# Performance work log

Hardware: AMD Instinct MI355X
Metric: run time of the kernel (lower is better)

The kernel has to match this reference:

```python
import jax, jax.numpy as jnp
import numpy as np
from jax import lax

ANCHOR_LENGTHS = (1.0, 2.0, 3.0, 4.0, 5.0, 7.0, 9.0)
B, C, LF = 8, 512, 8192
A = len(ANCHOR_LENGTHS)
PRE_K, POST_K = 600, 100          # pre/post NMS topk (propose defaults)
SCORE_TH, IOU_TH = 0.1, 0.5


def setup_inputs() -> dict:
    key = jax.random.key(0)
    ks = jax.random.split(key, 7)
    def n(k, shape, scale=1.0):
        return jax.random.normal(k, shape, dtype=jnp.float32) * scale
    return {
        "feat": n(ks[0], (B, C, LF)),
        "conv_w": n(ks[1], (C, C, 3), 0.02),
        "conv_b": n(ks[2], (C,), 0.02),
        "obj_w": n(ks[3], (A, C), 0.02),
        "obj_b": n(ks[4], (A,), 0.02),
        "reg_w": n(ks[5], (2 * A, C), 0.02),
        "reg_b": n(ks[6], (2 * A,), 0.02),
    }


def make_anchors_1d(Lf):
    lengths = jnp.asarray(ANCHOR_LENGTHS, jnp.float32)  # [A]
    centers = jnp.arange(Lf, dtype=jnp.float32) + 0.5   # [Lf]
    start = centers[:, None] - 0.5 * lengths[None, :]
    end = centers[:, None] + 0.5 * lengths[None, :]
    return jnp.stack([start, end], axis=-1).reshape(Lf * A, 2)  # [Lf*A, 2]


def decode_deltas_to_boxes(anchors, deltas, Lf):
    # anchors [N,2], deltas [B,N,2]
    a_c = 0.5 * (anchors[:, 0] + anchors[:, 1])
    a_w = jnp.clip(anchors[:, 1] - anchors[:, 0], 1e-6)
    t_c = deltas[..., 0]
    t_w = jnp.clip(deltas[..., 1], -10.0, 10.0)
    c = a_c[None, :] + t_c * a_w[None, :]
    w = a_w[None, :] * jnp.exp(t_w)
    Lff = jnp.float32(Lf)
    start = jnp.clip(c - 0.5 * w, 0.0, Lff)
    end = jnp.clip(c + 0.5 * w, 0.0, Lff)
    eps = 1e-3
    end = jnp.minimum(jnp.maximum(end, start + eps), Lff)
    start = jnp.maximum(jnp.minimum(start, end - eps), 0.0)
    return jnp.stack([start, end], axis=-1)  # [B,N,2]


def _nms_keep(boxes, valid):
    # boxes [K,2] already sorted by descending score; valid [K] bool
    s, e = boxes[:, 0], boxes[:, 1]
    inter = jnp.clip(jnp.minimum(e[:, None], e[None, :]) -
                     jnp.maximum(s[:, None], s[None, :]), 0.0)
    w = e - s
    union = w[:, None] + w[None, :] - inter
    iou = inter / jnp.clip(union, 1e-6)  # [K,K]; matches torchvision 2D trick (y-extent 1)
    idx = jnp.arange(boxes.shape[0])
    def body(i, keep):
        sup = jnp.any(keep & (idx < i) & (iou[i] > IOU_TH))
        return keep.at[i].set(keep[i] & jnp.logical_not(sup))
    return lax.fori_loop(0, boxes.shape[0], body, valid)


def propose(obj_logits, boxes):
    # fixed-shape, batched version of RPN1D.propose (no fallback path):
    # outputs are padded to POST_K with a validity mask.
    scores = jax.nn.sigmoid(obj_logits)                    # [B,N]
    s_top, idx = lax.top_k(scores, PRE_K)                  # sorted desc
    bxs = jnp.take_along_axis(boxes, idx[:, :, None], axis=1)  # [B,K,2]
    valid = s_top >= SCORE_TH
    keep = jax.vmap(_nms_keep)(bxs, valid)                 # [B,K]
    s_kept = jnp.where(keep, s_top, -1.0)
    s_out, j = lax.top_k(s_kept, POST_K)                   # kept, in score order
    b_out = jnp.take_along_axis(bxs, j[:, :, None], axis=1)
    vmask = s_out > 0.0
    return (jnp.where(vmask[:, :, None], b_out, 0.0),
            jnp.where(vmask, s_out, 0.0),
            vmask)


def reference(feat, conv_w, conv_b, obj_w, obj_b, reg_w, reg_b):
    # feat [B,C,Lf]; conv1d k=3 pad=1 + relu
    h = lax.conv_general_dilated(feat, conv_w, window_strides=(1,),
                                 padding=((1, 1),),
                                 dimension_numbers=("NCH", "OIH", "NCH"))
    h = jax.nn.relu(h + conv_b[None, :, None])
    x = jnp.transpose(h, (0, 2, 1))                        # [B,Lf,C]
    obj = jnp.einsum("blc,ac->bla", x, obj_w) + obj_b      # [B,Lf,A]
    reg = jnp.einsum("blc,ac->bla", x, reg_w) + reg_b      # [B,Lf,2A]
    Bsz, Lf = x.shape[0], x.shape[1]
    obj = obj.reshape(Bsz, Lf * A)                          # [B,N]
    reg = reg.reshape(Bsz, Lf * A, 2)                       # [B,N,2]
    anchors = make_anchors_1d(Lf)                           # [N,2]
    boxes = decode_deltas_to_boxes(anchors, reg, Lf)        # [B,N,2]
    props, pscores, pmask = propose(obj, boxes)
    return obj, reg, anchors, props, pscores, pmask
```

## Files before the change

### kernel.cpp

```cpp
#include <hip/hip_runtime.h>

#define LF 8192
#define NB 8
#define NC 512
#define NA 7
#define NANCH 57344
#define PRE_K 600
#define POST_K 100

#define OBJ_OFF   0
#define REG_OFF   458752
#define ANCH_OFF  1376256
#define PROPS_OFF 1490944
#define PSC_OFF   1492544
#define PM_OFF    1493344

#define WF_BYTES   3145728
#define GHIST_OFF  WF_BYTES
#define GHIST_BYTES (8 * 65536 * 4)

typedef __attribute__((ext_vector_type(8))) short bf16x8;
typedef __attribute__((ext_vector_type(4))) float f32x4;

__device__ __forceinline__ unsigned short f2bf(float f) {
  unsigned u = __float_as_uint(f);
  u += 0x7fff + ((u >> 16) & 1);
  return (unsigned short)(u >> 16);
}
__device__ __forceinline__ float bf2f(unsigned short h) {
  return __uint_as_float(((unsigned)h) << 16);
}

__device__ __forceinline__ void cvt_split(float v0, float v1,
                                          unsigned& hw, unsigned& lw) {
  asm("v_cvt_pk_bf16_f32 %0, %1, %2" : "=v"(hw) : "v"(v0), "v"(v1));
  float h0f = __uint_as_float(hw << 16);
  float h1f = __uint_as_float(hw & 0xffff0000u);
  asm("v_cvt_pk_bf16_f32 %0, %1, %2" : "=v"(lw) : "v"(v0 - h0f), "v"(v1 - h1f));
}

__global__ void prep_w_k(const float* __restrict__ cw, unsigned short* __restrict__ wf,
                         float* __restrict__ out, unsigned* __restrict__ ghist) {
  int o = blockIdx.x * 256 + threadIdx.x;
  {
    size_t z = 2 * (size_t)o;
    if (z < ANCH_OFF) {
      out[z] = 0.f;
      if (z + 1 < ANCH_OFF) out[z + 1] = 0.f;
    }
  }
  if (o < 8 * 65536) ghist[o] = 0u;
  if (o < NANCH) {
    int l = o / 7, a = o - l * 7;
    float len = (float)(a + 1 + (a > 4 ? a - 4 : 0));
    float c = (float)l + 0.5f;
    out[ANCH_OFF + 2 * (size_t)o]     = c - 0.5f * len;
    out[ANCH_OFF + 2 * (size_t)o + 1] = c + 0.5f * len;
  }
  if (o >= 786432) return;
  int j    = o & 7;
  int lane = (o >> 3) & 63;
  int cotl = (o >> 9) & 7;
  int rem  = o >> 12;
  int tap  = rem % 3;
  int cc   = rem / 3;
  int co = (cc >> 4) * 128 + cotl * 16 + (lane & 15);
  int ci = (cc & 15) * 32 + (lane >> 4) * 8 + j;
  float w = cw[((size_t)co * 512 + ci) * 3 + tap];
  unsigned short hi = f2bf(w);
  unsigned short lo = f2bf(w - bf2f(hi));
  size_t base = ((((size_t)rem * 8 + cotl) * 2) * 64 + lane) * 8 + j;
  wf[base] = hi;
  wf[base + 512] = lo;
}

#define BUFSH 10400
__global__ __launch_bounds__(256) void conv_proj_k(
    const float* __restrict__ feat, const unsigned short* __restrict__ wfrag,
    const float* __restrict__ cbias, const float* __restrict__ obj_w,
    const float* __restrict__ obj_b, const float* __restrict__ reg_w,
    const float* __restrict__ reg_b, float* __restrict__ out, int bbase)
{
  __shared__ __align__(16) char smem[41600];
  unsigned short* sb = (unsigned short*)smem;
  float* bufp = (float*)smem;

  const int tid  = threadIdx.x;
  const int l0   = blockIdx.x * 128;
  const int cob  = blockIdx.y;
  const int b    = bbase + blockIdx.z;
  const int lane = tid & 63, wave = tid >> 6;
  const int wm = wave >> 1, wn = wave & 1;
  const int quad = lane >> 4, l15 = lane & 15;

  const float* fb = feat + (size_t)b * 512 * LF;
  const bf16x8* wf8 = (const bf16x8*)wfrag;

  f32x4 acc[4][4];
  #pragma unroll
  for (int mt = 0; mt < 4; ++mt)
    #pragma unroll
    for (int nt = 0; nt < 4; ++nt) acc[mt][nt] = (f32x4){0.f, 0.f, 0.f, 0.f};

  const int r8 = tid & 7, cp2 = (tid >> 3) & 15, set = tid >> 7;

  const int brr = tid >> 4, bc2 = tid & 15;
  const int bl = (brr == 0) ? (l0 - 1) : (l0 + 128);
  const bool bok = (bl >= 0) && (bl < LF);

  float pv0[8], pv1[8], bv0 = 0.f, bv1 = 0.f;

  auto prefetch = [&](int ch) {
    const int cb = ch * 32;
    #pragma unroll
    for (int p = 0; p < 8; ++p) {
      int l = l0 + p * 16 + set * 8 + r8;
      pv0[p] = fb[(size_t)(cb + 2 * cp2) * LF + l];
      pv1[p] = fb[(size_t)(cb + 2 * cp2 + 1) * LF + l];
    }
    if (tid < 32 && bok) {
      bv0 = fb[(size_t)(cb + 2 * bc2) * LF + bl];
      bv1 = fb[(size_t)(cb + 2 * bc2 + 1) * LF + bl];
    }
  };
  auto stage = [&](int bi) {
    unsigned short* fh = sb + bi * BUFSH;
    unsigned short* fl = fh + 5200;
    #pragma unroll
    for (int p = 0; p < 8; ++p) {
      int row = p * 16 + set * 8 + r8;
      unsigned hw, lw;
      cvt_split(pv0[p], pv1[p], hw, lw);
      int e = (row + 1) * 40 + 2 * cp2;
      *(unsigned*)(fh + e) = hw;
      *(unsigned*)(fl + e) = lw;
    }
    if (tid < 32) {
      unsigned hw, lw;
      cvt_split(bv0, bv1, hw, lw);
      int e = (brr * 129) * 40 + 2 * bc2;
      *(unsigned*)(fh + e) = hw;
      *(unsigned*)(fl + e) = lw;
    }
  };

  prefetch(0);
  stage(0);
  prefetch(1);
  __syncthreads();

  for (int chunk = 0; chunk < 16; ++chunk) {
    const unsigned short* fh = sb + (chunk & 1) * BUFSH;
    const unsigned short* fl = fh + 5200;
    const int rem3 = (cob * 16 + chunk) * 3;

    bf16x8 AhA[4], AlA[4], AhB[4], AlB[4];
    bf16x8 Bh[4], Bl[4];

    auto loadA = [&](int tap, bf16x8* AH, bf16x8* AL) {
      #pragma unroll
      for (int mt = 0; mt < 4; ++mt) {
        int fi = (((rem3 + tap) * 8 + wm * 4 + mt) * 2) * 64 + lane;
        AH[mt] = wf8[fi];
        AL[mt] = wf8[fi + 64];
      }
    };
    auto loadB = [&](int tap) {
      #pragma unroll
      for (int nt = 0; nt < 4; ++nt) {
        int row = wn * 64 + nt * 16 + l15 + tap;
        int e = row * 40 + quad * 8;
        Bh[nt] = *(const bf16x8*)(fh + e);
        Bl[nt] = *(const bf16x8*)(fl + e);
      }
    };
    auto mfma_tap = [&](const bf16x8* AH, const bf16x8* AL) {
      __builtin_amdgcn_s_setprio(1);
      #pragma unroll
      for (int mt = 0; mt < 4; ++mt)
        #pragma unroll
        for (int nt = 0; nt < 4; ++nt) {
          acc[mt][nt] = __builtin_amdgcn_mfma_f32_16x16x32_bf16(AH[mt], Bh[nt], acc[mt][nt], 0, 0, 0);
          acc[mt][nt] = __builtin_amdgcn_mfma_f32_16x16x32_bf16(AH[mt], Bl[nt], acc[mt][nt], 0, 0, 0);
          acc[mt][nt] = __builtin_amdgcn_mfma_f32_16x16x32_bf16(AL[mt], Bh[nt], acc[mt][nt], 0, 0, 0);
        }
      __builtin_amdgcn_s_setprio(0);
    };

    loadA(0, AhA, AlA);
    if (chunk < 15) stage((chunk + 1) & 1);
    loadB(0);
    loadA(1, AhB, AlB);
    __builtin_amdgcn_sched_barrier(0);
    mfma_tap(AhA, AlA);
    loadB(1);
    loadA(2, AhA, AlA);
    __builtin_amdgcn_sched_barrier(0);
    mfma_tap(AhB, AlB);
    loadB(2);
    if (chunk < 14) prefetch(chunk + 2);
    mfma_tap(AhA, AlA);
    __syncthreads();
  }

  const int sg = tid >> 5;
  const int ll = tid & 31;
  int rc0 = 3 * sg     < 21 ? 3 * sg     : 20;
  int rc1 = 3 * sg + 1 < 21 ? 3 * sg + 1 : 20;
  int rc2 = 3 * sg + 2 < 21 ? 3 * sg + 2 : 20;
  const float* wr0 = (rc0 < 7) ? (obj_w + (size_t)rc0 * 512) : (reg_w + (size_t)(rc0 - 7) * 512);
  const float* wr1 = (rc1 < 7) ? (obj_w + (size_t)rc1 * 512) : (reg_w + (size_t)(rc1 - 7) * 512);
  const float* wr2 = (rc2 < 7) ? (obj_w + (size_t)rc2 * 512) : (reg_w + (size_t)(rc2 - 7) * 512);
  float pacc[3][4];
  #pragma unroll
  for (int q = 0; q < 3; ++q)
    #pragma unroll
    for (int m = 0; m < 4; ++m) pacc[q][m] = 0.f;

  #pragma unroll
  for (int h = 0; h < 2; ++h) {
    __syncthreads();
    if (wm == h) {
      #pragma unroll
      for (int mt = 0; mt < 4; ++mt) {
        f32x4 bv = *(const f32x4*)(cbias + cob * 128 + h * 64 + mt * 16 + quad * 4);
        #pragma unroll
        for (int nt = 0; nt < 4; ++nt) {
          int col = wn * 64 + nt * 16 + l15;
          #pragma unroll
          for (int r = 0; r < 4; ++r)
            bufp[(mt * 16 + quad * 4 + r) * 130 + col] = fmaxf(acc[mt][nt][r] + bv[r], 0.f);
        }
      }
    }
    __syncthreads();
    for (int c = 0; c < 64; ++c) {
      int cg = cob * 128 + h * 64 + c;
      float w0 = wr0[cg], w1 = wr1[cg], w2 = wr2[cg];
      #pragma unroll
      for (int m = 0; m < 4; ++m) {
        float hv = bufp[c * 130 + ll + 32 * m];
        pacc[0][m] = fmaf(w0, hv, pacc[0][m]);
        pacc[1][m] = fmaf(w1, hv, pacc[1][m]);
        pacc[2][m] = fmaf(w2, hv, pacc[2][m]);
      }
    }
  }

  const size_t ob = (size_t)b * NANCH;
  #pragma unroll
  for (int q = 0; q < 3; ++q) {
    int r = 3 * sg + q;
    if (r < 21) {
      #pragma unroll
      for (int m = 0; m < 4; ++m) {
        int l = l0 + ll + 32 * m;
        float v = pacc[q][m] + ((cob == 0) ? ((r < 7) ? obj_b[r] : reg_b[r - 7]) : 0.f);
        if (r < 7) atomicAdd(&out[OBJ_OFF + ob + (size_t)l * 7 + r], v);
        else { int rr = r - 7; atomicAdd(&out[REG_OFF + (ob + (size_t)l * 7 + (rr >> 1)) * 2 + (rr & 1)], v); }
      }
    }
  }
}

__device__ __forceinline__ unsigned keybits(float x) {
  unsigned u = __float_as_uint(x);
  return (u & 0x80000000u) ? ~u : (u | 0x80000000u);
}

__global__ __launch_bounds__(256) void hist_k(const float* __restrict__ out,
                                              unsigned* __restrict__ ghist) {
  const int b = blockIdx.y;
  const float* obj = out + OBJ_OFF + (size_t)b * NANCH;
  unsigned* h = ghist + (size_t)b * 65536;
  const int base = blockIdx.x * 256 + threadIdx.x;
  float v[8];
  #pragma unroll
  for (int k = 0; k < 8; ++k) v[k] = obj[base + k * 7168];
  #pragma unroll
  for (int k = 0; k < 8; ++k) {
    unsigned bin = keybits(v[k]) >> 16;
    unsigned phys = ((bin & 255u) << 8) | (bin >> 8);
    atomicAdd(&h[phys], 1u);
  }
}

__global__ __launch_bounds__(1024) void propose_k(float* __restrict__ out,
                                                  const unsigned* __restrict__ ghist) {
  const int b = blockIdx.x;
  const int tid = threadIdx.x;
  const int lane = tid & 63;
  const int wave = tid >> 6;

  __shared__ unsigned long long pool[PRE_K * 10];
  __shared__ unsigned part[1024];
  __shared__ unsigned coarse[256];
  __shared__ float bs[PRE_K], be[PRE_K], bsc[PRE_K];
  __shared__ unsigned long long vwords[10];
  __shared__ int scal[6];

  unsigned long long* keys = pool;
  const float* obj = out + OBJ_OFF + (size_t)b * NANCH;
  const unsigned* gh = ghist + (size_t)b * 65536;

  if (tid < 10) vwords[tid] = 0ull;
  if (tid == 0) scal[2] = 0;

  {
    const int q = tid >> 8, h8 = tid & 255;
    unsigned s = 0;
    #pragma unroll 8
    for (int lo = 0; lo < 64; ++lo) s += gh[((unsigned)(q * 64 + lo) << 8) | (unsigned)h8];
    part[tid] = s;
  }
  __syncthreads();
  if (tid < 256) coarse[tid] = part[tid] + part[tid + 256] + part[tid + 512] + part[tid + 768];
  __syncthreads();
  for (int off = 1; off < 256; off <<= 1) {
    unsigned v = 0, add = 0;
    if (tid < 256) { v = coarse[tid]; add = (tid + off < 256) ? coarse[tid + off] : 0u; }
    __syncthreads();
    if (tid < 256) coarse[tid] = v + add;
    __syncthreads();
  }
  if (tid < 256) {
    unsigned sfx  = coarse[tid];
    unsigned sfx1 = (tid < 255) ? coarse[tid + 1] : 0u;
    if (sfx >= (unsigned)PRE_K && sfx1 < (unsigned)PRE_K) { scal[0] = tid; scal[1] = (int)sfx1; }
  }
  __syncthreads();
  const int hi8 = scal[0];
  const int before1 = scal[1];
  __syncthreads();
  if (tid < 256) coarse[tid] = gh[((unsigned)tid << 8) | (unsigned)hi8];
  __syncthreads();
  for (int off = 1; off < 256; off <<= 1) {
    unsigned v = 0, add = 0;
    if (tid < 256) { v = coarse[tid]; add = (tid + off < 256) ? coarse[tid + off] : 0u; }
    __syncthreads();
    if (tid < 256) coarse[tid] = v + add;
    __syncthreads();
  }
  if (tid < 256) {
    unsigned sfx  = coarse[tid];
    unsigned sfx1 = (tid < 255) ? coarse[tid + 1] : 0u;
    if (before1 + (int)sfx >= PRE_K && before1 + (int)sfx1 < PRE_K) scal[4] = tid;
  }
  __syncthreads();
  const unsigned Tbits = ((((unsigned)hi8 << 8) | (unsigned)scal[4]) << 16);

  for (int it = 0; it < 7; ++it) {
    float v[8];
    #pragma unroll
    for (int k = 0; k < 8; ++k) v[k] = obj[it * 8192 + k * 1024 + tid];
    #pragma unroll
    for (int k = 0; k < 8; ++k) {
      unsigned u = keybits(v[k]);
      if (u >= Tbits) {
        int p = atomicAdd(&scal[2], 1);
        if (p < 1024)
          keys[p] = ((unsigned long long)u << 32) |
                    (unsigned long long)(~(unsigned)(it * 8192 + k * 1024 + tid));
      }
    }
  }
  __syncthreads();
  const int cnt = scal[2];
  if (tid >= cnt) keys[tid] = 0ull;
  for (unsigned k = 2; k <= 1024; k <<= 1) {
    for (unsigned j = k >> 1; j > 0; j >>= 1) {
      __syncthreads();
      unsigned idx = tid, partner = idx ^ j;
      if (partner > idx) {
        unsigned long long a = keys[idx], c = keys[partner];
        bool up = ((idx & k) == 0);
        if (up ? (a < c) : (a > c)) { keys[idx] = c; keys[partner] = a; }
      }
    }
  }
  __syncthreads();
  if (tid < PRE_K) {
    const int t = tid;
    unsigned long long kv = keys[t];
    unsigned u  = (unsigned)(kv >> 32);
    unsigned i2 = ~((unsigned)kv);
    unsigned ub = (u & 0x80000000u) ? (u & 0x7fffffffu) : ~u;
    float logit = __uint_as_float(ub);
    float score = 1.f / (1.f + expf(-logit));
    int li = (int)(i2 / 7u);
    int a  = (int)(i2 - (unsigned)li * 7u);
    float alen = (float)(a + 1 + (a > 4 ? a - 4 : 0));
    const float* rp = out + REG_OFF + ((size_t)b * NANCH + i2) * 2;
    float tc = rp[0];
    float tw = fminf(fmaxf(rp[1], -10.f), 10.f);
    float cc = (float)li + 0.5f + tc * alen;
    float ww = alen * expf(tw);
    float s0 = cc - 0.5f * ww;
    float e0 = cc + 0.5f * ww;
    s0 = fminf(fmaxf(s0, 0.f), (float)LF);
    e0 = fminf(fmaxf(e0, 0.f), (float)LF);
    e0 = fminf(fmaxf(e0, s0 + 1e-3f), (float)LF);
    s0 = fmaxf(fminf(s0, e0 - 1e-3f), 0.f);
    bs[t] = s0; be[t] = e0; bsc[t] = score;
    if (score >= 0.1f) atomicOr(&vwords[t >> 6], 1ull << (t & 63));
  }
  __syncthreads();
  for (int widx = tid; widx < PRE_K * 10; widx += 1024) {
    int j = widx / 10;
    int w = widx - j * 10;
    int base = w * 64;
    unsigned long long m = 0ull;
    if (base + 63 > j) {
      float sj = bs[j], ej = be[j];
      float wj = ej - sj;
      for (int bit = 0; bit < 64; ++bit) {
        int i3 = base + bit;
        if (i3 > j && i3 < PRE_K) {
          float inter = fmaxf(fminf(ej, be[i3]) - fmaxf(sj, bs[i3]), 0.f);
          float uni = wj + (be[i3] - bs[i3]) - inter;
          float iou = inter / fmaxf(uni, 1e-6f);
          if (iou > 0.5f) m |= (1ull << bit);
        }
      }
    }
    pool[widx] = m;
  }
  __syncthreads();
  if (wave == 0) {
    unsigned long long rem = 0ull;
    unsigned long long vw = (lane < 10) ? vwords[lane] : 0ull;
    unsigned long long mrow = (lane < 10) ? pool[lane] : 0ull;
    int kept = 0;
    for (int i3 = 0; i3 < PRE_K; ++i3) {
      unsigned long long mnext =
          (lane < 10 && (i3 + 1) < PRE_K) ? pool[(i3 + 1) * 10 + lane] : 0ull;
      unsigned long long avail = vw & ~rem;
      unsigned long long ow = __shfl(avail, i3 >> 6);
      if ((ow >> (i3 & 63)) & 1ull) {
        rem |= mrow;
        if (lane == 0) {
          out[PROPS_OFF + (size_t)b * 200 + 2 * kept]     = bs[i3];
          out[PROPS_OFF + (size_t)b * 200 + 2 * kept + 1] = be[i3];
          out[PSC_OFF + (size_t)b * 100 + kept] = bsc[i3];
          out[PM_OFF  + (size_t)b * 100 + kept] = 1.0f;
        }
        ++kept;
        if (kept >= POST_K) break;
      }
      mrow = mnext;
    }
    if (lane == 0) scal[3] = kept;
  }
  __syncthreads();
  const int kf = scal[3];
  if (tid < POST_K && tid >= kf) {
    out[PROPS_OFF + (size_t)b * 200 + 2 * tid]     = 0.f;
    out[PROPS_OFF + (size_t)b * 200 + 2 * tid + 1] = 0.f;
    out[PSC_OFF + (size_t)b * 100 + tid] = 0.f;
    out[PM_OFF  + (size_t)b * 100 + tid] = 0.f;
  }
}

extern "C" void kernel_launch(void* const* d_in, const int* in_sizes, int n_in,
                              void* d_out, int out_size, void* d_ws, size_t ws_size,
                              hipStream_t stream) {
  const float* feat = (const float*)d_in[0];
  const float* cw   = (const float*)d_in[1];
  const float* cb   = (const float*)d_in[2];
  const float* ow   = (const float*)d_in[3];
  const float* obb  = (const float*)d_in[4];
  const float* rw   = (const float*)d_in[5];
  const float* rb   = (const float*)d_in[6];
  float* out = (float*)d_out;
  unsigned short* wf = (unsigned short*)d_ws;
  unsigned* ghist = (unsigned*)((char*)d_ws + GHIST_OFF);

  hipLaunchKernelGGL(prep_w_k, dim3(3072), dim3(256), 0, stream, cw, wf, out, ghist);
  hipLaunchKernelGGL(conv_proj_k, dim3(64, 4, 4), dim3(256), 0, stream,
                     feat, wf, cb, ow, obb, rw, rb, out, 0);
  hipLaunchKernelGGL(conv_proj_k, dim3(64, 4, 4), dim3(256), 0, stream,
                     feat, wf, cb, ow, obb, rw, rb, out, 4);
  hipLaunchKernelGGL(hist_k, dim3(28, 8), dim3(256), 0, stream, out, ghist);
  hipLaunchKernelGGL(propose_k, dim3(8), dim3(1024), 0, stream, out, ghist);
}
```

Before: 634.0 us.

## Remap conv MFMA wave tiling to 128x32 per wave with split-M A loads

Each wave now computes all 128 output channels over a 32-column slice of L, instead of a 64x64 quadrant. B fragments from LDS are halved per wave while the A (weight) fragments loaded from global memory double, and the A loads are split into two half-M blocks that are interleaved with the MFMA calls. The epilogue is adjusted so that every wave writes its rows for each half. The intent is to cut LDS traffic and allow finer load/compute overlap, at the cost of more global or L2 weight reads per wave.

```diff
diff --git a/kernel.cpp b/kernel.cpp
--- a/kernel.cpp
+++ b/kernel.cpp
@@ -90,17 +90,16 @@
   const int cob  = blockIdx.y;
   const int b    = bbase + blockIdx.z;
   const int lane = tid & 63, wave = tid >> 6;
-  const int wm = wave >> 1, wn = wave & 1;
   const int quad = lane >> 4, l15 = lane & 15;
 
   const float* fb = feat + (size_t)b * 512 * LF;
   const bf16x8* wf8 = (const bf16x8*)wfrag;
 
-  f32x4 acc[4][4];
-  #pragma unroll
-  for (int mt = 0; mt < 4; ++mt)
-    #pragma unroll
-    for (int nt = 0; nt < 4; ++nt) acc[mt][nt] = (f32x4){0.f, 0.f, 0.f, 0.f};
+  f32x4 acc[8][2];
+  #pragma unroll
+  for (int mt = 0; mt < 8; ++mt)
+    #pragma unroll
+    for (int nt = 0; nt < 2; ++nt) acc[mt][nt] = (f32x4){0.f, 0.f, 0.f, 0.f};
 
   const int r8 = tid & 7, cp2 = (tid >> 3) & 15, set = tid >> 7;
 
@@ -155,51 +154,60 @@
     const int rem3 = (cob * 16 + chunk) * 3;
 
     bf16x8 AhA[4], AlA[4], AhB[4], AlB[4];
-    bf16x8 Bh[4], Bl[4];
-
-    auto loadA = [&](int tap, bf16x8* AH, bf16x8* AL) {
-      #pragma unroll
-      for (int mt = 0; mt < 4; ++mt) {
-        int fi = (((rem3 + tap) * 8 + wm * 4 + mt) * 2) * 64 + lane;
-        AH[mt] = wf8[fi];
-        AL[mt] = wf8[fi + 64];
+    bf16x8 Bh[2], Bl[2];
+
+    auto loadA = [&](int tap, int mh, bf16x8* AH, bf16x8* AL) {
+      #pragma unroll
+      for (int mt2 = 0; mt2 < 4; ++mt2) {
+        int fi = (((rem3 + tap) * 8 + mh * 4 + mt2) * 2) * 64 + lane;
+        AH[mt2] = wf8[fi];
+        AL[mt2] = wf8[fi + 64];
       }
     };
     auto loadB = [&](int tap) {
       #pragma unroll
-      for (int nt = 0; nt < 4; ++nt) {
-        int row = wn * 64 + nt * 16 + l15 + tap;
+      for (int nt = 0; nt < 2; ++nt) {
+        int row = wave * 32 + nt * 16 + l15 + tap;
         int e = row * 40 + quad * 8;
         Bh[nt] = *(const bf16x8*)(fh + e);
         Bl[nt] = *(const bf16x8*)(fl + e);
       }
     };
-    auto mfma_tap = [&](const bf16x8* AH, const bf16x8* AL) {
+    auto mfma_blk = [&](int mh, const bf16x8* AH, const bf16x8* AL) {
       __builtin_amdgcn_s_setprio(1);
       #pragma unroll
-      for (int mt = 0; mt < 4; ++mt)
+      for (int mt2 = 0; mt2 < 4; ++mt2)
         #pragma unroll
-        for (int nt = 0; nt < 4; ++nt) {
-          acc[mt][nt] = __builtin_amdgcn_mfma_f32_16x16x32_bf16(AH[mt], Bh[nt], acc[mt][nt], 0, 0, 0);
-          acc[mt][nt] = __builtin_amdgcn_mfma_f32_16x16x32_bf16(AH[mt], Bl[nt], acc[mt][nt], 0, 0, 0);
-          acc[mt][nt] = __builtin_amdgcn_mfma_f32_16x16x32_bf16(AL[mt], Bh[nt], acc[mt][nt], 0, 0, 0);
+        for (int nt = 0; nt < 2; ++nt) {
+          acc[mh * 4 + mt2][nt] = __builtin_amdgcn_mfma_f32_16x16x32_bf16(AH[mt2], Bh[nt], acc[mh * 4 + mt2][nt], 0, 0, 0);
+          acc[mh * 4 + mt2][nt] = __builtin_amdgcn_mfma_f32_16x16x32_bf16(AH[mt2], Bl[nt], acc[mh * 4 + mt2][nt], 0, 0, 0);
+          acc[mh * 4 + mt2][nt] = __builtin_amdgcn_mfma_f32_16x16x32_bf16(AL[mt2], Bh[nt], acc[mh * 4 + mt2][nt], 0, 0, 0);
         }
       __builtin_amdgcn_s_setprio(0);
     };
 
-    loadA(0, AhA, AlA);
+    loadA(0, 0, AhA, AlA);
     if (chunk < 15) stage((chunk + 1) & 1);
     loadB(0);
-    loadA(1, AhB, AlB);
+    loadA(0, 1, AhB, AlB);
     __builtin_amdgcn_sched_barrier(0);
-    mfma_tap(AhA, AlA);
+    mfma_blk(0, AhA, AlA);
+    loadA(1, 0, AhA, AlA);
+    __builtin_amdgcn_sched_barrier(0);
+    mfma_blk(1, AhB, AlB);
     loadB(1);
-    loadA(2, AhA, AlA);
+    loadA(1, 1, AhB, AlB);
     __builtin_amdgcn_sched_barrier(0);
-    mfma_tap(AhB, AlB);
+    mfma_blk(0, AhA, AlA);
+    loadA(2, 0, AhA, AlA);
+    __builtin_amdgcn_sched_barrier(0);
+    mfma_blk(1, AhB, AlB);
     loadB(2);
+    loadA(2, 1, AhB, AlB);
     if (chunk < 14) prefetch(chunk + 2);
-    mfma_tap(AhA, AlA);
+    __builtin_amdgcn_sched_barrier(0);
+    mfma_blk(0, AhA, AlA);
+    mfma_blk(1, AhB, AlB);
     __syncthreads();
   }
 
@@ -220,17 +228,15 @@
   #pragma unroll
   for (int h = 0; h < 2; ++h) {
     __syncthreads();
-    if (wm == h) {
-      #pragma unroll
-      for (int mt = 0; mt < 4; ++mt) {
-        f32x4 bv = *(const f32x4*)(cbias + cob * 128 + h * 64 + mt * 16 + quad * 4);
+    #pragma unroll
+    for (int mt2 = 0; mt2 < 4; ++mt2) {
+      f32x4 bv = *(const f32x4*)(cbias + cob * 128 + h * 64 + mt2 * 16 + quad * 4);
+      #pragma unroll
+      for (int nt = 0; nt < 2; ++nt) {
+        int col = wave * 32 + nt * 16 + l15;
         #pragma unroll
-        for (int nt = 0; nt < 4; ++nt) {
-          int col = wn * 64 + nt * 16 + l15;
-          #pragma unroll
-          for (int r = 0; r < 4; ++r)
-            bufp[(mt * 16 + quad * 4 + r) * 130 + col] = fmaxf(acc[mt][nt][r] + bv[r], 0.f);
-        }
+        for (int r = 0; r < 4; ++r)
+          bufp[(mt2 * 16 + quad * 4 + r) * 130 + col] = fmaxf(acc[h * 4 + mt2][nt][r] + bv[r], 0.f);
       }
     }
     __syncthreads();
```

After: 669.0 us. 5.5% more time.
